# Optimization experiments

Measured on AMD Instinct MI355X. Metric: run time of the kernel, lower is better.

The kernel has to match this reference:

```python
import jax, jax.numpy as jnp
import numpy as np

H, KVH, DH = 32, 8, 128        # attention heads, kv heads, head dim (shared by both streams)
G = H // KVH                   # GQA group size
EPS = 1e-6


def rms_norm(x, w):
    xf = x.astype(jnp.float32)
    n = xf * jax.lax.rsqrt(jnp.mean(xf * xf, axis=-1, keepdims=True) + EPS)
    return (n * w).astype(x.dtype)


def apply_rope(x, positions, max_wavelength=10000.0):
    # x: [B, L, h, DH], positions: [B, L]
    d_half = x.shape[-1] // 2
    freq_exponents = (2.0 / x.shape[-1]) * jnp.arange(d_half, dtype=jnp.float32)
    timescale = max_wavelength ** freq_exponents
    radians = positions[..., None].astype(jnp.float32) / timescale          # [B, L, d_half]
    radians = radians[..., None, :]                                         # [B, L, 1, d_half]
    s, c = jnp.sin(radians), jnp.cos(radians)
    xf = x.astype(jnp.float32)
    x1, x2 = xf[..., :d_half], xf[..., d_half:]
    out = jnp.concatenate([x1 * c - x2 * s, x2 * c + x1 * s], axis=-1)
    return out.astype(x.dtype)


def setup_inputs() -> dict:
    key = jax.random.key(0)
    ks = jax.random.split(key, 16)
    B, LV, LE = 2, 1024, 64
    DV, DE = 2560, 1920
    s = 0.02
    inp = {
        "vlm_embeds": jax.random.normal(ks[0], (B, LV, DV), jnp.float32),
        "expert_embeds": jax.random.normal(ks[1], (B, LE, DE), jnp.float32),
        "position_ids": jnp.sort(jax.random.randint(ks[2], (B, LV + LE), 0, 2048), axis=-1),
        "attention_mask": jnp.ones((B, LV + LE, LV + LE), dtype=bool),
        "w_ln_vlm": jnp.ones((DV,), jnp.float32),
        "Wq_vlm": jax.random.normal(ks[3], (DV, H * DH), jnp.float32) * s,
        "Wk_vlm": jax.random.normal(ks[4], (DV, KVH * DH), jnp.float32) * s,
        "Wv_vlm": jax.random.normal(ks[5], (DV, KVH * DH), jnp.float32) * s,
        "Wo_vlm": jax.random.normal(ks[6], (H * DH, DV), jnp.float32) * s,
        "w_ln_exp": jnp.ones((DE,), jnp.float32),
        "Wq_exp": jax.random.normal(ks[7], (DE, H * DH), jnp.float32) * s,
        "Wk_exp": jax.random.normal(ks[8], (DE, KVH * DH), jnp.float32) * s,
        "Wv_exp": jax.random.normal(ks[9], (DE, KVH * DH), jnp.float32) * s,
        "Wo_exp": jax.random.normal(ks[10], (H * DH, DE), jnp.float32) * s,
    }
    return inp


def _mixed_attn_layer(vlm_embeds, expert_embeds,
                      w_ln_vlm, Wq_vlm, Wk_vlm, Wv_vlm, Wo_vlm,
                      w_ln_exp, Wq_exp, Wk_exp, Wv_exp, Wo_exp,
                      position_ids, attention_mask, knowledge_insulation=True):
    B, LV, _ = vlm_embeds.shape
    LE = expert_embeds.shape[1]

    # Stream 0: VLM prefix (knowledge insulation -> no grad into VLM path).
    hv = rms_norm(vlm_embeds, w_ln_vlm)
    qv = (hv @ Wq_vlm).reshape(B, LV, H, DH)
    kv = (hv @ Wk_vlm).reshape(B, LV, KVH, DH)
    vv = (hv @ Wv_vlm).reshape(B, LV, KVH, DH)
    if knowledge_insulation:
        qv = jax.lax.stop_gradient(qv)
        kv = jax.lax.stop_gradient(kv)
        vv = jax.lax.stop_gradient(vv)

    # Stream 1: expert suffix.
    he = rms_norm(expert_embeds, w_ln_exp)
    qe = (he @ Wq_exp).reshape(B, LE, H, DH)
    ke = (he @ Wk_exp).reshape(B, LE, KVH, DH)
    ve = (he @ Wv_exp).reshape(B, LE, KVH, DH)

    # Concatenate streams along the sequence dim, then inline RoPE on q and k.
    q = jnp.concatenate([qv, qe], axis=1)          # [B, L, 32, 128]
    k = jnp.concatenate([kv, ke], axis=1)          # [B, L, 8, 128]
    v = jnp.concatenate([vv, ve], axis=1)
    q = apply_rope(q, position_ids)
    k = apply_rope(k, position_ids)

    # Eager GQA attention in fp32 (matches _eager_attention_forward).
    k_full = jnp.repeat(k, G, axis=2)              # kv-head major, group minor
    v_full = jnp.repeat(v, G, axis=2)
    att = jnp.einsum("bqhd,bkhd->bhqk", q.astype(jnp.float32), k_full.astype(jnp.float32))
    att = att * (DH ** -0.5)
    big_neg = jnp.finfo(jnp.float32).min
    att = jnp.where(attention_mask[:, None, :, :], att, big_neg)
    probs = jax.nn.softmax(att, axis=-1).astype(v_full.dtype)
    out = jnp.einsum("bhqk,bkhd->bqhd", probs, v_full).reshape(B, LV + LE, H * DH)

    # Split back to streams, per-stream output projection + residual.
    out_vlm = vlm_embeds + out[:, :LV] @ Wo_vlm
    out_exp = expert_embeds + out[:, LV:] @ Wo_exp
    return out_vlm, out_exp


def reference(vlm_embeds, expert_embeds, position_ids, attention_mask,
              w_ln_vlm, Wq_vlm, Wk_vlm, Wv_vlm, Wo_vlm,
              w_ln_exp, Wq_exp, Wk_exp, Wv_exp, Wo_exp):
    _, out_exp = _mixed_attn_layer(
        vlm_embeds, expert_embeds,
        w_ln_vlm, Wq_vlm, Wk_vlm, Wv_vlm, Wo_vlm,
        w_ln_exp, Wq_exp, Wk_exp, Wv_exp, Wo_exp,
        position_ids, attention_mask)
    return out_exp
```

## Files before the change

### kernel.cpp

```cpp
#include <hip/hip_runtime.h>
#include <hip/hip_bf16.h>
#include <cstddef>

#define B_  2
#define LV_ 1024
#define LE_ 64
#define S_TOT 1088
#define DV_ 2560
#define DE_ 1920
#define H_  32
#define KVH_ 8
#define DH_ 128
#define HD_ 4096
#define KVD_ 1024
#define NSPL 17

typedef short short8 __attribute__((ext_vector_type(8)));
typedef float f32x4 __attribute__((ext_vector_type(4)));

typedef __hip_bfloat16 bf16;

__device__ inline float b2f(bf16 h) { return __bfloat162float(h); }
__device__ inline bf16 f2b(float f) { return __float2bfloat16(f); }

typedef const __attribute__((address_space(1))) void* gptr_t;
typedef __attribute__((address_space(3))) void* lptr_t;
__device__ inline void gl16(const void* g, void* l) {
  __builtin_amdgcn_global_load_lds((gptr_t)g, (lptr_t)l, 16, 0, 0);
}

#define OFF_HVB   0ul
#define OFF_WKVT  10485760ul
#define OFF_HEB   20971520ul
#define OFF_WQKVT 21463040ul
#define OFF_QE    45056000ul
#define OFF_KBUF  46104576ul
#define OFF_VBUF  50561024ul
#define OFF_AO    59473920ul
#define OFF_OP    0ul
#define OFF_M     35651584ul
#define OFF_L     35930112ul

__global__ __launch_bounds__(256) void rmsnorm_both(
    const float* __restrict__ xv, const float* __restrict__ wv,
    bf16* __restrict__ ov,
    const float* __restrict__ xe, const float* __restrict__ we,
    bf16* __restrict__ oe) {
  int row; const float* x; const float* w; bf16* o; int D;
  if (blockIdx.x < 2048) { row = blockIdx.x;        x = xv; w = wv; o = ov; D = DV_; }
  else                   { row = blockIdx.x - 2048; x = xe; w = we; o = oe; D = DE_; }
  const float4* x4 = (const float4*)(x + (size_t)row * D);
  const float4* w4 = (const float4*)w;
  int D4 = D >> 2;
  float ss = 0.f;
  for (int i = threadIdx.x; i < D4; i += 256) {
    float4 v = x4[i];
    ss += v.x * v.x + v.y * v.y + v.z * v.z + v.w * v.w;
  }
  __shared__ float red[256];
  red[threadIdx.x] = ss; __syncthreads();
  for (int s = 128; s > 0; s >>= 1) {
    if (threadIdx.x < s) red[threadIdx.x] += red[threadIdx.x + s];
    __syncthreads();
  }
  float inv = rsqrtf(red[0] / (float)D + 1e-6f);
  ushort4* o4 = (ushort4*)(o + (size_t)row * D);
  for (int i = threadIdx.x; i < D4; i += 256) {
    float4 v = x4[i], wv2 = w4[i];
    bf16 a = f2b(v.x * inv * wv2.x), b = f2b(v.y * inv * wv2.y);
    bf16 c = f2b(v.z * inv * wv2.z), d = f2b(v.w * inv * wv2.w);
    ushort4 ow;
    ow.x = *(ushort*)&a; ow.y = *(ushort*)&b; ow.z = *(ushort*)&c; ow.w = *(ushort*)&d;
    o4[i] = ow;
  }
}

__device__ inline void tile_tconv(float (*t)[65],
    const float* __restrict__ W, bf16* __restrict__ Wt,
    int K, int N, int n_off, int bx, int by) {
  int n0 = bx * 64, k0 = by * 64;
  int tid = threadIdx.x;
  int c = tid & 63, r4 = tid >> 6;
#pragma unroll 4
  for (int it = 0; it < 16; ++it) {
    int k = it * 4 + r4;
    t[k][c] = W[(size_t)(k0 + k) * N + n0 + c];
  }
  __syncthreads();
#pragma unroll 4
  for (int it = 0; it < 16; ++it) {
    int n = it * 4 + r4;
    Wt[(size_t)(n_off + n0 + n) * K + k0 + c] = f2b(t[c][n]);
  }
}

__global__ __launch_bounds__(256) void tconv_all(
    const float* __restrict__ Wk_vlm, const float* __restrict__ Wv_vlm,
    const float* __restrict__ Wq_exp, const float* __restrict__ Wk_exp,
    const float* __restrict__ Wv_exp,
    bf16* __restrict__ WkvT, bf16* __restrict__ WqkvT) {
  __shared__ float t[64][65];
  int id = blockIdx.x;
  if (id < 640)       tile_tconv(t, Wk_vlm, WkvT, DV_, KVD_, 0,    id % 16, id / 16);
  else if (id < 1280) { id -= 640;  tile_tconv(t, Wv_vlm, WkvT,  DV_, KVD_, 1024, id % 16, id / 16); }
  else if (id < 3200) { id -= 1280; tile_tconv(t, Wq_exp, WqkvT, DE_, HD_,  0,    id % 64, id / 64); }
  else if (id < 3680) { id -= 3200; tile_tconv(t, Wk_exp, WqkvT, DE_, KVD_, 4096, id % 16, id / 16); }
  else                { id -= 3680; tile_tconv(t, Wv_exp, WqkvT, DE_, KVD_, 5120, id % 16, id / 16); }
}

__global__ __launch_bounds__(256) void gemm_fused(
    const bf16* __restrict__ hv, const bf16* __restrict__ WkvT,
    const bf16* __restrict__ he, const bf16* __restrict__ WqkvT,
    bf16* __restrict__ kbuf, bf16* __restrict__ vbuf, bf16* __restrict__ qe) {
  __shared__ ushort As[4][64][32];
  __shared__ ushort Bs[4][128][32];
  int tid = threadIdx.x;
  int lane = tid & 63, w = tid >> 6;
  int lr = lane & 15, quad = lane >> 4;
  int wmA = (w >> 1) * 32, wnB = (w & 1) * 64;

  bool expert = (blockIdx.x >= 512);
  const ushort* Ab; const ushort* Bb; int K, nsteps, m0, n0;
  if (!expert) {
    m0 = (int)(blockIdx.x >> 4) * 64; n0 = (int)(blockIdx.x & 15) * 128;
    Ab = (const ushort*)hv; Bb = (const ushort*)WkvT;
    K = DV_; nsteps = DV_ / 32;
  } else {
    int e = (int)blockIdx.x - 512;
    m0 = (e / 48) * 64; n0 = (e % 48) * 128;
    Ab = (const ushort*)he; Bb = (const ushort*)WqkvT;
    K = DE_; nsteps = DE_ / 32;
  }

  int rA  = w * 16 + (lane >> 2);
  int rB0 = w * 32 + (lane >> 2);
  int rB1 = rB0 + 16;
  int sA  = (lane & 3) ^ ((rA  >> 1) & 3);
  int sB0 = (lane & 3) ^ ((rB0 >> 1) & 3);
  int sB1 = (lane & 3) ^ ((rB1 >> 1) & 3);
  const ushort* pa  = Ab + (size_t)(m0 + rA)  * K + sA  * 8;
  const ushort* pb0 = Bb + (size_t)(n0 + rB0) * K + sB0 * 8;
  const ushort* pb1 = Bb + (size_t)(n0 + rB1) * K + sB1 * 8;

  auto STAGE = [&](int buf, int t) {
    int k0 = t * 32;
    gl16(pa  + k0, &As[buf][w * 16][0]);
    gl16(pb0 + k0, &Bs[buf][w * 32][0]);
    gl16(pb1 + k0, &Bs[buf][w * 32 + 16][0]);
  };

  int sslot = (quad ^ ((lr >> 1) & 3)) * 8;

  f32x4 acc[2][4] = {};

  STAGE(0, 0);
  STAGE(1, 1);
  STAGE(2, 2);
  for (int t = 0; t < nsteps; ++t) {
    int rem = nsteps - t;
    if (rem > 3) {
      STAGE((t + 3) & 3, t + 3);
      asm volatile("s_waitcnt vmcnt(9)" ::: "memory");
    } else if (rem == 3) {
      asm volatile("s_waitcnt vmcnt(6)" ::: "memory");
    } else if (rem == 2) {
      asm volatile("s_waitcnt vmcnt(3)" ::: "memory");
    } else {
      asm volatile("s_waitcnt vmcnt(0)" ::: "memory");
    }
    __builtin_amdgcn_s_barrier();

    int cur = t & 3;
    short8 af[2], bv[4];
#pragma unroll
    for (int i = 0; i < 2; ++i)
      af[i] = *(const short8*)&As[cur][wmA + i * 16 + lr][sslot];
#pragma unroll
    for (int j = 0; j < 4; ++j)
      bv[j] = *(const short8*)&Bs[cur][wnB + j * 16 + lr][sslot];
    __builtin_amdgcn_s_setprio(1);
#pragma unroll
    for (int i = 0; i < 2; ++i)
#pragma unroll
      for (int j = 0; j < 4; ++j)
        acc[i][j] = __builtin_amdgcn_mfma_f32_16x16x32_bf16(af[i], bv[j], acc[i][j], 0, 0, 0);
    __builtin_amdgcn_s_setprio(0);

    __builtin_amdgcn_s_barrier();
  }

#pragma unroll
  for (int i = 0; i < 2; ++i) {
    int mm_base = wmA + i * 16 + quad * 4;
#pragma unroll
    for (int j = 0; j < 4; ++j) {
      int gn = n0 + wnB + j * 16 + lr;
#pragma unroll
      for (int r = 0; r < 4; ++r) {
        int mm = mm_base + r;
        float v = acc[i][j][r];
        if (!expert) {
          int m = m0 + mm;
          int b = m >> 10, s = m & 1023;
          size_t row = (size_t)(b * S_TOT + s);
          if (gn < 1024) kbuf[row * KVD_ + gn] = f2b(v);
          else           vbuf[row * KVD_ + (gn - 1024)] = f2b(v);
        } else {
          int m = m0 + mm;
          int b = m >> 6, l = m & 63;
          if (gn < 4096) {
            qe[(size_t)m * HD_ + gn] = f2b(v);
          } else {
            size_t row = (size_t)(b * S_TOT + LV_ + l);
            if (gn < 5120) kbuf[row * KVD_ + (gn - 4096)] = f2b(v);
            else           vbuf[row * KVD_ + (gn - 5120)] = f2b(v);
          }
        }
      }
    }
  }
}

__global__ __launch_bounds__(256) void gemm_out(
    const bf16* __restrict__ A, const float* __restrict__ W,
    float* __restrict__ out) {
  __shared__ ushort As[128][40];
  __shared__ ushort Bs[64][40];
  int tid = threadIdx.x;
  int lane = tid & 63, wid = tid >> 6;
  int wm = (wid >> 1) * 64, wn = (wid & 1) * 32;
  int n0 = blockIdx.x * 64;
  int k_beg = blockIdx.y * 256;
  int lr = lane & 15, quad = lane >> 4;

  f32x4 acc[4][2] = {};

  int ar = tid >> 2;
  int ac = (tid & 3) * 8;
  const ushort* Aptr = (const ushort*)A + (size_t)ar * HD_ + ac;
  int bn = tid & 63, kg = tid >> 6;
  int bslot_w = ((kg ^ (bn & 3)) * 8);
  int brd = (quad ^ (lr & 3)) * 8;

  for (int k0 = k_beg; k0 < k_beg + 256; k0 += 32) {
    short8 a0 = *(const short8*)(Aptr + k0);
    short8 a1 = *(const short8*)(Aptr + (size_t)64 * HD_ + k0);
    float wv[8];
#pragma unroll
    for (int j = 0; j < 8; ++j)
      wv[j] = W[(size_t)(k0 + kg * 8 + j) * DE_ + n0 + bn];
    short8 bvv;
#pragma unroll
    for (int j = 0; j < 8; ++j) { bf16 h = f2b(wv[j]); bvv[j] = *(short*)&h; }
    __syncthreads();
    *(short8*)&As[ar][ac] = a0;
    *(short8*)&As[64 + ar][ac] = a1;
    *(short8*)&Bs[bn][bslot_w] = bvv;
    __syncthreads();
    short8 af[4], bfr[2];
#pragma unroll
    for (int i = 0; i < 4; ++i)
      af[i]  = *(const short8*)&As[wm + i * 16 + lr][quad * 8];
#pragma unroll
    for (int j = 0; j < 2; ++j)
      bfr[j] = *(const short8*)&Bs[wn + j * 16 + lr][brd];
#pragma unroll
    for (int i = 0; i < 4; ++i)
#pragma unroll
      for (int j = 0; j < 2; ++j)
        acc[i][j] = __builtin_amdgcn_mfma_f32_16x16x32_bf16(af[i], bfr[j], acc[i][j], 0, 0, 0);
  }

#pragma unroll
  for (int i = 0; i < 4; ++i) {
    int m_base = wm + i * 16 + quad * 4;
#pragma unroll
    for (int j = 0; j < 2; ++j) {
      int gn = n0 + wn + j * 16 + lr;
#pragma unroll
      for (int r = 0; r < 4; ++r)
        atomicAdd(&out[(size_t)(m_base + r) * 1920 + gn], acc[i][j][r]);
    }
  }
}

__global__ __launch_bounds__(256) void rope_fused(
    bf16* __restrict__ qe, bf16* __restrict__ kbuf,
    const int* __restrict__ pos_ids) {
  if (blockIdx.x < 128) {
    int row = blockIdx.x;
    int b = row >> 6, l = row & 63;
    float pos = (float)pos_ids[b * S_TOT + LV_ + l];
    bf16* qrow = qe + (size_t)row * HD_;
    for (int p = threadIdx.x; p < H_ * 64; p += 256) {
      int hh = p >> 6, i = p & 63;
      float inv_ts = expf(-9.210340371976184f * (float)i * (1.0f / 64.0f));
      float r = pos * inv_ts;
      float sn = sinf(r), cs = cosf(r);
      float x1 = b2f(qrow[hh * DH_ + i]), x2 = b2f(qrow[hh * DH_ + i + 64]);
      qrow[hh * DH_ + i]      = f2b(x1 * cs - x2 * sn);
      qrow[hh * DH_ + i + 64] = f2b(x2 * cs + x1 * sn);
    }
  } else {
    int bid = blockIdx.x - 128;
    int s = bid % S_TOT, b = bid / S_TOT;
    float pos = (float)pos_ids[b * S_TOT + s];
    size_t base = ((size_t)(b * S_TOT + s)) * KVD_;
    for (int t = threadIdx.x; t < KVH_ * 64; t += 256) {
      int kvh = t >> 6, i = t & 63;
      size_t idx = base + kvh * DH_ + i;
      float inv_ts = expf(-9.210340371976184f * (float)i * (1.0f / 64.0f));
      float r = pos * inv_ts;
      float sn = sinf(r), cs = cosf(r);
      float x1 = b2f(kbuf[idx]), x2 = b2f(kbuf[idx + 64]);
      kbuf[idx]      = f2b(x1 * cs - x2 * sn);
      kbuf[idx + 64] = f2b(x2 * cs + x1 * sn);
    }
  }
}

__global__ __launch_bounds__(256) void attn_part(
    const bf16* __restrict__ qe, const bf16* __restrict__ kbuf,
    const bf16* __restrict__ vbuf,
    float* __restrict__ O_p, float* __restrict__ m_arr,
    float* __restrict__ l_arr) {
  int bh = blockIdx.x & 63;
  int split = blockIdx.x >> 6;
  int h = bh & 31, b = bh >> 5;
  int kvh = h >> 2;
  int tid = threadIdx.x;
  int lane = tid & 63, wid = tid >> 6;
  int lr = lane & 15, quad = lane >> 4;

  __shared__ ushort Ks[64][152];
  __shared__ ushort vTs[128][72];
  __shared__ ushort sc[4][16][72];

  short8 qf[4];
  {
    const ushort* qptr = (const ushort*)qe +
        ((size_t)(b * LE_ + wid * 16 + lr)) * HD_ + h * DH_ + quad * 8;
#pragma unroll
    for (int ks = 0; ks < 4; ++ks) qf[ks] = *(const short8*)(qptr + ks * 32);
  }

  f32x4 Of[8] = {};
  float m_i[4], l_i[4];

  const float scale = 0.08838834764831845f;
  int key0 = split * 64;

  {
    int dg = tid & 15, kq = tid >> 4;
#pragma unroll
    for (int it = 0; it < 4; ++it) {
      int key = it * 16 + kq;
      short8 v = *(const short8*)((const ushort*)kbuf +
          ((size_t)(b * S_TOT + key0 + key) * KVH_ + kvh) * DH_ + dg * 8);
      *(short8*)&Ks[key][dg * 8] = v;
    }
  }
  {
    int key = tid & 63, dgrp = tid >> 6;
    const ushort* vp = (const ushort*)vbuf +
        ((size_t)(b * S_TOT + key0 + key) * KVH_ + kvh) * DH_ + dgrp * 32;
    short8 vv[4];
#pragma unroll
    for (int q8 = 0; q8 < 4; ++q8) vv[q8] = *(const short8*)(vp + q8 * 8);
#pragma unroll
    for (int q8 = 0; q8 < 4; ++q8)
#pragma unroll
      for (int j = 0; j < 8; ++j)
        vTs[dgrp * 32 + q8 * 8 + j][key] = (ushort)vv[q8][j];
  }
  __syncthreads();

  f32x4 Sf[4] = {};
#pragma unroll
  for (int kt = 0; kt < 4; ++kt)
#pragma unroll
    for (int ks = 0; ks < 4; ++ks) {
      short8 kf = *(const short8*)&Ks[kt * 16 + lr][quad * 8 + ks * 32];
      Sf[kt] = __builtin_amdgcn_mfma_f32_16x16x32_bf16(qf[ks], kf, Sf[kt], 0, 0, 0);
    }

#pragma unroll
  for (int kt = 0; kt < 4; ++kt) Sf[kt] *= scale;
#pragma unroll
  for (int r = 0; r < 4; ++r) {
    float mx = fmaxf(fmaxf(Sf[0][r], Sf[1][r]), fmaxf(Sf[2][r], Sf[3][r]));
#pragma unroll
    for (int msk = 1; msk < 16; msk <<= 1) mx = fmaxf(mx, __shfl_xor(mx, msk));
    m_i[r] = mx;
    float ls = 0.f;
#pragma unroll
    for (int kt = 0; kt < 4; ++kt) {
      float p = __expf(Sf[kt][r] - mx);
      Sf[kt][r] = p;
      ls += p;
    }
    l_i[r] = ls;
#pragma unroll
    for (int kt = 0; kt < 4; ++kt) {
      bf16 t = f2b(Sf[kt][r]);
      sc[wid][quad * 4 + r][kt * 16 + lr] = *(ushort*)&t;
    }
  }

#pragma unroll
  for (int ks = 0; ks < 2; ++ks) {
    short8 pf = *(const short8*)&sc[wid][lr][quad * 8 + ks * 32];
#pragma unroll
    for (int nt = 0; nt < 8; ++nt) {
      short8 vf = *(const short8*)&vTs[nt * 16 + lr][quad * 8 + ks * 32];
      Of[nt] = __builtin_amdgcn_mfma_f32_16x16x32_bf16(pf, vf, Of[nt], 0, 0, 0);
    }
  }

  float l_row[4];
#pragma unroll
  for (int r = 0; r < 4; ++r) {
    float l = l_i[r];
#pragma unroll
    for (int msk = 1; msk < 16; msk <<= 1) l += __shfl_xor(l, msk);
    l_row[r] = l;
  }

  size_t rbase = (size_t)split * 4096 + (size_t)bh * 64;
#pragma unroll
  for (int nt = 0; nt < 8; ++nt)
#pragma unroll
    for (int r = 0; r < 4; ++r) {
      int q = wid * 16 + quad * 4 + r;
      O_p[(rbase + q) * 128 + nt * 16 + lr] = Of[nt][r];
    }
  if (lr == 0) {
#pragma unroll
    for (int r = 0; r < 4; ++r) {
      int q = wid * 16 + quad * 4 + r;
      m_arr[rbase + q] = m_i[r];
      l_arr[rbase + q] = l_row[r];
    }
  }
}

__global__ __launch_bounds__(256) void attn_combine(
    const float* __restrict__ O_p, const float* __restrict__ m_arr,
    const float* __restrict__ l_arr, bf16* __restrict__ ao) {
  int t = blockIdx.x * 256 + threadIdx.x;
  int d = t & 127, row = t >> 7;
  float m_g = -1e30f;
#pragma unroll
  for (int s = 0; s < NSPL; ++s) m_g = fmaxf(m_g, m_arr[s * 4096 + row]);
  float denom = 0.f, acc = 0.f;
#pragma unroll
  for (int s = 0; s < NSPL; ++s) {
    float w = __expf(m_arr[s * 4096 + row] - m_g);
    denom += w * l_arr[s * 4096 + row];
    acc   += w * O_p[((size_t)s * 4096 + row) * 128 + d];
  }
  int b = row >> 11, h = (row >> 6) & 31, q = row & 63;
  bf16 o = f2b(acc / denom);
  ((ushort*)ao)[((size_t)(b * 64 + q) * 32 + h) * 128 + d] = *(ushort*)&o;
}

extern "C" void kernel_launch(void* const* d_in, const int* in_sizes, int n_in,
                              void* d_out, int out_size, void* d_ws, size_t ws_size,
                              hipStream_t stream) {
  const float* vlm      = (const float*)d_in[0];
  const float* expe     = (const float*)d_in[1];
  const int*   pos      = (const int*)d_in[2];
  const float* w_ln_vlm = (const float*)d_in[4];
  const float* Wk_vlm   = (const float*)d_in[6];
  const float* Wv_vlm   = (const float*)d_in[7];
  const float* w_ln_exp = (const float*)d_in[9];
  const float* Wq_exp   = (const float*)d_in[10];
  const float* Wk_exp   = (const float*)d_in[11];
  const float* Wv_exp   = (const float*)d_in[12];
  const float* Wo_exp   = (const float*)d_in[13];
  float* out = (float*)d_out;
  char* ws = (char*)d_ws;

  bf16* hv_b  = (bf16*)(ws + OFF_HVB);
  bf16* WkvT  = (bf16*)(ws + OFF_WKVT);
  bf16* he_b  = (bf16*)(ws + OFF_HEB);
  bf16* WqkvT = (bf16*)(ws + OFF_WQKVT);
  bf16* qe    = (bf16*)(ws + OFF_QE);
  bf16* kbuf  = (bf16*)(ws + OFF_KBUF);
  bf16* vbuf  = (bf16*)(ws + OFF_VBUF);
  bf16* ao    = (bf16*)(ws + OFF_AO);
  float* O_p   = (float*)(ws + OFF_OP);
  float* m_arr = (float*)(ws + OFF_M);
  float* l_arr = (float*)(ws + OFF_L);

  hipMemcpyAsync(out, expe, (size_t)B_ * LE_ * DE_ * sizeof(float),
                 hipMemcpyDeviceToDevice, stream);

  rmsnorm_both<<<B_ * LV_ + B_ * LE_, 256, 0, stream>>>(
      vlm, w_ln_vlm, hv_b, expe, w_ln_exp, he_b);

  tconv_all<<<4160, 256, 0, stream>>>(Wk_vlm, Wv_vlm, Wq_exp, Wk_exp, Wv_exp,
                                      WkvT, WqkvT);

  gemm_fused<<<608, 256, 0, stream>>>(hv_b, WkvT, he_b, WqkvT, kbuf, vbuf, qe);

  rope_fused<<<128 + B_ * S_TOT, 256, 0, stream>>>(qe, kbuf, pos);

  attn_part<<<64 * NSPL, 256, 0, stream>>>(qe, kbuf, vbuf, O_p, m_arr, l_arr);
  attn_combine<<<4096 * 128 / 256, 256, 0, stream>>>(O_p, m_arr, l_arr, ao);

  gemm_out<<<dim3(30, 16), 256, 0, stream>>>(ao, Wo_exp, out);
}
```

Before: 306.5 us.

## Shrink projection GEMM tiles and process two key chunks per attention split

The fused QKV projection GEMM moves from 64x128 tiles with a 4-stage LDS pipeline to 64x64 tiles with 3 stages, doubling the grid to 1216 blocks. This is meant to raise occupancy and CU coverage, at the cost of less operand reuse per block. Attention splits drop from 17 to 9, each handling two 64-key chunks with an online-softmax rescale. That halves the partial outputs written and the work left for the combine kernel, in exchange for fewer attention blocks and serial work inside each one.

```diff
diff --git a/kernel.cpp b/kernel.cpp
--- a/kernel.cpp
+++ b/kernel.cpp
@@ -13,7 +13,7 @@
 #define DH_ 128
 #define HD_ 4096
 #define KVD_ 1024
-#define NSPL 17
+#define NSPL 9
 
 typedef short short8 __attribute__((ext_vector_type(8)));
 typedef float f32x4 __attribute__((ext_vector_type(4)));
@@ -38,8 +38,8 @@
 #define OFF_VBUF  50561024ul
 #define OFF_AO    59473920ul
 #define OFF_OP    0ul
-#define OFF_M     35651584ul
-#define OFF_L     35930112ul
+#define OFF_M     18874368ul
+#define OFF_L     19021824ul
 
 __global__ __launch_bounds__(256) void rmsnorm_both(
     const float* __restrict__ xv, const float* __restrict__ wv,
@@ -112,89 +112,81 @@
     const bf16* __restrict__ hv, const bf16* __restrict__ WkvT,
     const bf16* __restrict__ he, const bf16* __restrict__ WqkvT,
     bf16* __restrict__ kbuf, bf16* __restrict__ vbuf, bf16* __restrict__ qe) {
-  __shared__ ushort As[4][64][32];
-  __shared__ ushort Bs[4][128][32];
+  __shared__ ushort As[3][64][32];
+  __shared__ ushort Bs[3][64][32];
   int tid = threadIdx.x;
   int lane = tid & 63, w = tid >> 6;
   int lr = lane & 15, quad = lane >> 4;
-  int wmA = (w >> 1) * 32, wnB = (w & 1) * 64;
-
-  bool expert = (blockIdx.x >= 512);
+  int wm = (w >> 1) * 32, wn = (w & 1) * 32;
+
+  bool expert = (blockIdx.x >= 1024);
   const ushort* Ab; const ushort* Bb; int K, nsteps, m0, n0;
   if (!expert) {
-    m0 = (int)(blockIdx.x >> 4) * 64; n0 = (int)(blockIdx.x & 15) * 128;
+    m0 = (int)(blockIdx.x >> 5) * 64; n0 = (int)(blockIdx.x & 31) * 64;
     Ab = (const ushort*)hv; Bb = (const ushort*)WkvT;
     K = DV_; nsteps = DV_ / 32;
   } else {
-    int e = (int)blockIdx.x - 512;
-    m0 = (e / 48) * 64; n0 = (e % 48) * 128;
+    int e = (int)blockIdx.x - 1024;
+    m0 = (e / 96) * 64; n0 = (e % 96) * 64;
     Ab = (const ushort*)he; Bb = (const ushort*)WqkvT;
     K = DE_; nsteps = DE_ / 32;
   }
 
-  int rA  = w * 16 + (lane >> 2);
-  int rB0 = w * 32 + (lane >> 2);
-  int rB1 = rB0 + 16;
-  int sA  = (lane & 3) ^ ((rA  >> 1) & 3);
-  int sB0 = (lane & 3) ^ ((rB0 >> 1) & 3);
-  int sB1 = (lane & 3) ^ ((rB1 >> 1) & 3);
-  const ushort* pa  = Ab + (size_t)(m0 + rA)  * K + sA  * 8;
-  const ushort* pb0 = Bb + (size_t)(n0 + rB0) * K + sB0 * 8;
-  const ushort* pb1 = Bb + (size_t)(n0 + rB1) * K + sB1 * 8;
+  int rr = w * 16 + (lane >> 2);
+  int ss = (lane & 3) ^ ((rr >> 1) & 3);
+  const ushort* pa = Ab + (size_t)(m0 + rr) * K + ss * 8;
+  const ushort* pb = Bb + (size_t)(n0 + rr) * K + ss * 8;
 
   auto STAGE = [&](int buf, int t) {
     int k0 = t * 32;
-    gl16(pa  + k0, &As[buf][w * 16][0]);
-    gl16(pb0 + k0, &Bs[buf][w * 32][0]);
-    gl16(pb1 + k0, &Bs[buf][w * 32 + 16][0]);
+    gl16(pa + k0, &As[buf][w * 16][0]);
+    gl16(pb + k0, &Bs[buf][w * 16][0]);
   };
 
   int sslot = (quad ^ ((lr >> 1) & 3)) * 8;
 
-  f32x4 acc[2][4] = {};
+  f32x4 acc[2][2] = {};
 
   STAGE(0, 0);
   STAGE(1, 1);
-  STAGE(2, 2);
+  int cur = 0, nxt = 2;
   for (int t = 0; t < nsteps; ++t) {
     int rem = nsteps - t;
-    if (rem > 3) {
-      STAGE((t + 3) & 3, t + 3);
-      asm volatile("s_waitcnt vmcnt(9)" ::: "memory");
-    } else if (rem == 3) {
-      asm volatile("s_waitcnt vmcnt(6)" ::: "memory");
+    if (rem > 2) {
+      STAGE(nxt, t + 2);
+      asm volatile("s_waitcnt vmcnt(4)" ::: "memory");
     } else if (rem == 2) {
-      asm volatile("s_waitcnt vmcnt(3)" ::: "memory");
+      asm volatile("s_waitcnt vmcnt(2)" ::: "memory");
     } else {
       asm volatile("s_waitcnt vmcnt(0)" ::: "memory");
     }
     __builtin_amdgcn_s_barrier();
 
-    int cur = t & 3;
-    short8 af[2], bv[4];
+    short8 af[2], bv[2];
+#pragma unroll
+    for (int i = 0; i < 2; ++i) {
+      af[i] = *(const short8*)&As[cur][wm + i * 16 + lr][sslot];
+      bv[i] = *(const short8*)&Bs[cur][wn + i * 16 + lr][sslot];
+    }
+    __builtin_amdgcn_s_setprio(1);
 #pragma unroll
     for (int i = 0; i < 2; ++i)
-      af[i] = *(const short8*)&As[cur][wmA + i * 16 + lr][sslot];
-#pragma unroll
-    for (int j = 0; j < 4; ++j)
-      bv[j] = *(const short8*)&Bs[cur][wnB + j * 16 + lr][sslot];
-    __builtin_amdgcn_s_setprio(1);
-#pragma unroll
-    for (int i = 0; i < 2; ++i)
-#pragma unroll
-      for (int j = 0; j < 4; ++j)
+#pragma unroll
+      for (int j = 0; j < 2; ++j)
         acc[i][j] = __builtin_amdgcn_mfma_f32_16x16x32_bf16(af[i], bv[j], acc[i][j], 0, 0, 0);
     __builtin_amdgcn_s_setprio(0);
 
     __builtin_amdgcn_s_barrier();
+    cur = (cur == 2) ? 0 : cur + 1;
+    nxt = (nxt == 2) ? 0 : nxt + 1;
   }
 
 #pragma unroll
   for (int i = 0; i < 2; ++i) {
-    int mm_base = wmA + i * 16 + quad * 4;
-#pragma unroll
-    for (int j = 0; j < 4; ++j) {
-      int gn = n0 + wnB + j * 16 + lr;
+    int mm_base = wm + i * 16 + quad * 4;
+#pragma unroll
+    for (int j = 0; j < 2; ++j) {
+      int gn = n0 + wn + j * 16 + lr;
 #pragma unroll
       for (int r = 0; r < 4; ++r) {
         int mm = mm_base + r;
@@ -346,74 +338,84 @@
 
   f32x4 Of[8] = {};
   float m_i[4], l_i[4];
+#pragma unroll
+  for (int r = 0; r < 4; ++r) { m_i[r] = -1e30f; l_i[r] = 0.f; }
 
   const float scale = 0.08838834764831845f;
-  int key0 = split * 64;
-
-  {
-    int dg = tid & 15, kq = tid >> 4;
-#pragma unroll
-    for (int it = 0; it < 4; ++it) {
-      int key = it * 16 + kq;
-      short8 v = *(const short8*)((const ushort*)kbuf +
-          ((size_t)(b * S_TOT + key0 + key) * KVH_ + kvh) * DH_ + dg * 8);
-      *(short8*)&Ks[key][dg * 8] = v;
-    }
-  }
-  {
-    int key = tid & 63, dgrp = tid >> 6;
-    const ushort* vp = (const ushort*)vbuf +
-        ((size_t)(b * S_TOT + key0 + key) * KVH_ + kvh) * DH_ + dgrp * 32;
-    short8 vv[4];
-#pragma unroll
-    for (int q8 = 0; q8 < 4; ++q8) vv[q8] = *(const short8*)(vp + q8 * 8);
-#pragma unroll
-    for (int q8 = 0; q8 < 4; ++q8)
-#pragma unroll
-      for (int j = 0; j < 8; ++j)
-        vTs[dgrp * 32 + q8 * 8 + j][key] = (ushort)vv[q8][j];
-  }
-  __syncthreads();
-
-  f32x4 Sf[4] = {};
-#pragma unroll
-  for (int kt = 0; kt < 4; ++kt)
-#pragma unroll
-    for (int ks = 0; ks < 4; ++ks) {
-      short8 kf = *(const short8*)&Ks[kt * 16 + lr][quad * 8 + ks * 32];
-      Sf[kt] = __builtin_amdgcn_mfma_f32_16x16x32_bf16(qf[ks], kf, Sf[kt], 0, 0, 0);
-    }
-
-#pragma unroll
-  for (int kt = 0; kt < 4; ++kt) Sf[kt] *= scale;
-#pragma unroll
-  for (int r = 0; r < 4; ++r) {
-    float mx = fmaxf(fmaxf(Sf[0][r], Sf[1][r]), fmaxf(Sf[2][r], Sf[3][r]));
-#pragma unroll
-    for (int msk = 1; msk < 16; msk <<= 1) mx = fmaxf(mx, __shfl_xor(mx, msk));
-    m_i[r] = mx;
-    float ls = 0.f;
-#pragma unroll
-    for (int kt = 0; kt < 4; ++kt) {
-      float p = __expf(Sf[kt][r] - mx);
-      Sf[kt][r] = p;
-      ls += p;
-    }
-    l_i[r] = ls;
-#pragma unroll
-    for (int kt = 0; kt < 4; ++kt) {
-      bf16 t = f2b(Sf[kt][r]);
-      sc[wid][quad * 4 + r][kt * 16 + lr] = *(ushort*)&t;
-    }
-  }
-
-#pragma unroll
-  for (int ks = 0; ks < 2; ++ks) {
-    short8 pf = *(const short8*)&sc[wid][lr][quad * 8 + ks * 32];
-#pragma unroll
-    for (int nt = 0; nt < 8; ++nt) {
-      short8 vf = *(const short8*)&vTs[nt * 16 + lr][quad * 8 + ks * 32];
-      Of[nt] = __builtin_amdgcn_mfma_f32_16x16x32_bf16(pf, vf, Of[nt], 0, 0, 0);
+  int nch = (split == 8) ? 1 : 2;
+
+  for (int c = 0; c < nch; ++c) {
+    int key0 = split * 128 + c * 64;
+    __syncthreads();
+    {
+      int dg = tid & 15, kq = tid >> 4;
+#pragma unroll
+      for (int it = 0; it < 4; ++it) {
+        int key = it * 16 + kq;
+        short8 v = *(const short8*)((const ushort*)kbuf +
+            ((size_t)(b * S_TOT + key0 + key) * KVH_ + kvh) * DH_ + dg * 8);
+        *(short8*)&Ks[key][dg * 8] = v;
+      }
+    }
+    {
+      int key = tid & 63, dgrp = tid >> 6;
+      const ushort* vp = (const ushort*)vbuf +
+          ((size_t)(b * S_TOT + key0 + key) * KVH_ + kvh) * DH_ + dgrp * 32;
+      short8 vv[4];
+#pragma unroll
+      for (int q8 = 0; q8 < 4; ++q8) vv[q8] = *(const short8*)(vp + q8 * 8);
+#pragma unroll
+      for (int q8 = 0; q8 < 4; ++q8)
+#pragma unroll
+        for (int j = 0; j < 8; ++j)
+          vTs[dgrp * 32 + q8 * 8 + j][key] = (ushort)vv[q8][j];
+    }
+    __syncthreads();
+
+    f32x4 Sf[4] = {};
+#pragma unroll
+    for (int kt = 0; kt < 4; ++kt)
+#pragma unroll
+      for (int ks = 0; ks < 4; ++ks) {
+        short8 kf = *(const short8*)&Ks[kt * 16 + lr][quad * 8 + ks * 32];
+        Sf[kt] = __builtin_amdgcn_mfma_f32_16x16x32_bf16(qf[ks], kf, Sf[kt], 0, 0, 0);
+      }
+
+#pragma unroll
+    for (int kt = 0; kt < 4; ++kt) Sf[kt] *= scale;
+#pragma unroll
+    for (int r = 0; r < 4; ++r) {
+      float mx = fmaxf(fmaxf(Sf[0][r], Sf[1][r]), fmaxf(Sf[2][r], Sf[3][r]));
+#pragma unroll
+      for (int msk = 1; msk < 16; msk <<= 1) mx = fmaxf(mx, __shfl_xor(mx, msk));
+      float mn = fmaxf(m_i[r], mx);
+      float alpha = __expf(m_i[r] - mn);
+      m_i[r] = mn;
+      float ls = 0.f;
+#pragma unroll
+      for (int kt = 0; kt < 4; ++kt) {
+        float p = __expf(Sf[kt][r] - mn);
+        Sf[kt][r] = p;
+        ls += p;
+      }
+      l_i[r] = l_i[r] * alpha + ls;
+#pragma unroll
+      for (int nt = 0; nt < 8; ++nt) Of[nt][r] *= alpha;
+#pragma unroll
+      for (int kt = 0; kt < 4; ++kt) {
+        bf16 t = f2b(Sf[kt][r]);
+        sc[wid][quad * 4 + r][kt * 16 + lr] = *(ushort*)&t;
+      }
+    }
+
+#pragma unroll
+    for (int ks = 0; ks < 2; ++ks) {
+      short8 pf = *(const short8*)&sc[wid][lr][quad * 8 + ks * 32];
+#pragma unroll
+      for (int nt = 0; nt < 8; ++nt) {
+        short8 vf = *(const short8*)&vTs[nt * 16 + lr][quad * 8 + ks * 32];
+        Of[nt] = __builtin_amdgcn_mfma_f32_16x16x32_bf16(pf, vf, Of[nt], 0, 0, 0);
+      }
     }
   }
 
@@ -502,7 +504,7 @@
   tconv_all<<<4160, 256, 0, stream>>>(Wk_vlm, Wv_vlm, Wq_exp, Wk_exp, Wv_exp,
                                       WkvT, WqkvT);
 
-  gemm_fused<<<608, 256, 0, stream>>>(hv_b, WkvT, he_b, WqkvT, kbuf, vbuf, qe);
+  gemm_fused<<<1216, 256, 0, stream>>>(hv_b, WkvT, he_b, WqkvT, kbuf, vbuf, qe);
 
   rope_fused<<<128 + B_ * S_TOT, 256, 0, stream>>>(qe, kbuf, pos);
 
```

Result: no change. 304.4 us (-0.7%).
